# Performance work log

Measured on AMD Instinct MI355X. Metric: run time of the kernel, lower is better.

The kernel has to match this reference:

```python
import jax, jax.numpy as jnp
from jax import lax
import numpy as np

T, B, I, H, O = 1000, 256, 128, 512, 32
ALPHA = 20.0 / 100.0  # dt / tau
EXC_RATIO = 0.8
SPARSITY = 0.2


def setup_inputs() -> dict:
    key = jax.random.key(0)
    ks = jax.random.split(key, 8)
    x = jax.random.normal(ks[0], (T, B, I), dtype=jnp.float32)
    w_in = jax.random.normal(ks[1], (H, I), dtype=jnp.float32) * (1.0 / np.sqrt(I))
    b_in = jax.random.uniform(ks[2], (H,), dtype=jnp.float32, minval=-1, maxval=1) / np.sqrt(I)
    w_h = jax.random.normal(ks[3], (H, H), dtype=jnp.float32) * (1.0 / np.sqrt(H))
    b_h = jax.random.uniform(ks[4], (H,), dtype=jnp.float32, minval=-1, maxval=1) / np.sqrt(H)
    n_exc = int(H * EXC_RATIO)
    dale = jnp.where(jnp.arange(H) < n_exc, 1.0, -1.0).astype(jnp.float32)
    # sparse mask: rand < sparsity, diagonal forced True
    sp = (jax.random.uniform(ks[5], (H, H)) < SPARSITY).astype(jnp.float32)
    sparse = jnp.maximum(sp, jnp.eye(H, dtype=jnp.float32))
    fc_w = jax.random.normal(ks[6], (O, H), dtype=jnp.float32) * (1.0 / np.sqrt(H))
    fc_b = jax.random.uniform(ks[7], (O,), dtype=jnp.float32, minval=-1, maxval=1) / np.sqrt(H)
    return {"x": x, "w_in": w_in, "b_in": b_in, "w_h": w_h, "b_h": b_h,
            "dale": dale, "sparse": sparse, "fc_w": fc_w, "fc_b": fc_b}


def reference(x, w_in, b_in, w_h, b_h, dale, sparse, fc_w, fc_b):
    alpha = jnp.float32(ALPHA)
    oma = jnp.float32(1.0 - ALPHA)
    # effective recurrent weight: relu(W) * dale (per presynaptic column) * sparse mask
    w_eff = jax.nn.relu(w_h) * dale[None, :] * sparse  # [H, H]
    # precompute input drive for all timesteps: [T, B, H]
    x_drive = jnp.einsum('tbi,hi->tbh', x, w_in) + b_in

    def step(carry, xd_t):
        state, out = carry
        total = xd_t + out @ w_eff.T + b_h  # [B, H]
        state = state * oma + total * alpha
        out = jax.nn.relu(state)
        return (state, out), out

    init = (jnp.zeros((B, H), x.dtype), jnp.zeros((B, H), x.dtype))
    _, rnn_activity = lax.scan(step, init, x_drive)  # [T, B, H]
    out = jnp.einsum('tbh,oh->tbo', rnn_activity, fc_w) + fc_b  # [T, B, O]
    return out, rnn_activity
```

## Files before the change

### kernel.cpp

```cpp
#include <hip/hip_runtime.h>

#define T_STEPS 1000
#define BATCH   256
#define IN_DIM  128
#define HID     512
#define OUT_DIM 32
#define ALPHA_F 0.2f
#define OMA_F   0.8f
#define MAXNNZ  96


__global__ __launch_bounds__(512) void build_rank_kernel(
    const float* __restrict__ w_h, const float* __restrict__ sparse,
    unsigned int* __restrict__ perm, unsigned int* __restrict__ nnzR)
{
    int tid = threadIdx.x;
    __shared__ int cnt_sh[HID];

    const float4* wr4 = (const float4*)(w_h    + tid * HID);
    const float4* sr4 = (const float4*)(sparse + tid * HID);
    int cnt = 0;
    for (int j4 = 0; j4 < HID / 4; j4++) {
        float4 w = wr4[j4];
        float4 s = sr4[j4];
        if (w.x > 0.f && s.x > 0.5f) cnt++;
        if (w.y > 0.f && s.y > 0.5f) cnt++;
        if (w.z > 0.f && s.z > 0.5f) cnt++;
        if (w.w > 0.f && s.w > 0.5f) cnt++;
    }
    int c = min(cnt, MAXNNZ);

    cnt_sh[tid] = c;
    __syncthreads();
    int rank = 0;
    for (int j = 0; j < HID; j++) {
        int cj = cnt_sh[j];
        rank += (cj < c) || (cj == c && j < tid);
    }
    perm[rank] = (unsigned int)tid;
    nnzR[rank] = (unsigned int)c;
}

__global__ __launch_bounds__(64) void fill_kernel(
    const float* __restrict__ w_h, const float* __restrict__ dale,
    const float* __restrict__ sparse,
    const unsigned int* __restrict__ perm, const unsigned int* __restrict__ nnzR,
    float* __restrict__ val_t, unsigned short* __restrict__ idx_t)
{
    int r    = blockIdx.x;
    int lane = threadIdx.x;
    int h = (int)perm[r];
    int c = (int)nnzR[r];

    float*          vout = val_t + r * MAXNNZ;
    unsigned short* iout = idx_t + r * MAXNNZ;

    for (int k = lane; k < MAXNNZ; k += 64)
        if (k >= c) { vout[k] = 0.f; iout[k] = 0; }

    unsigned long long lt = (1ull << lane) - 1ull;
    int pos_base = 0;
#pragma unroll
    for (int ch = 0; ch < 8; ch++) {
        int j = ch * 64 + lane;
        float w = w_h[h * HID + j];
        float s = sparse[h * HID + j];
        bool pred = (w > 0.f) && (s > 0.5f);
        unsigned long long m = __ballot(pred);
        if (pred) {
            int pos = pos_base + (int)__popcll(m & lt);
            if (pos < MAXNNZ) {
                vout[pos] = w * dale[j];
                iout[pos] = (unsigned short)(j * 4);
            }
        }
        pos_base += (int)__popcll(m);
    }
}

__global__ __launch_bounds__(256) void trans_kernel(
    const float* __restrict__ w_in, const float* __restrict__ fc_w,
    float* __restrict__ w_inT, float* __restrict__ fcT)
{
    int o = blockIdx.x * 256 + threadIdx.x;
    if (o < IN_DIM * HID) {
        int k = o / HID, n = o % HID;
        w_inT[o] = w_in[n * IN_DIM + k];
    } else {
        int o2 = o - IN_DIM * HID;
        if (o2 < HID * OUT_DIM) {
            int k = o2 / OUT_DIM, oo = o2 % OUT_DIM;
            fcT[o2] = fc_w[oo * HID + k];
        }
    }
}

__global__ __launch_bounds__(256, 4) void ingemm_kernel(
    const float* __restrict__ x, const float* __restrict__ w_inT,
    const float* __restrict__ b_in, const float* __restrict__ b_h,
    float* __restrict__ xd)
{
    __shared__ float xl[256 * 33];
    int tid = threadIdx.x;
    int B  = blockIdx.x;
    int r8 = B & 7;
    int tt = B >> 3;
    int nc = tt & 15;
    int aa = tt >> 4;
    int mb = 8 * aa + r8;
    long m0 = (long)mb * 256;
    int n0 = nc * 32;

    float acc[32];
#pragma unroll
    for (int j = 0; j < 32; j++) acc[j] = b_in[n0 + j] + b_h[n0 + j];

    for (int k0 = 0; k0 < IN_DIM; k0 += 32) {
        __syncthreads();
#pragma unroll
        for (int i = 0; i < 8; i++) {
            int f  = tid + i * 256;
            int rr = f >> 3, cc = f & 7;
            float4 v = *(const float4*)(x + (m0 + rr) * IN_DIM + k0 + cc * 4);
            float* d = &xl[rr * 33 + cc * 4];
            d[0] = v.x; d[1] = v.y; d[2] = v.z; d[3] = v.w;
        }
        __syncthreads();
        const float* xrow = &xl[tid * 33];
#pragma unroll
        for (int kk = 0; kk < 32; kk++) {
            float a = xrow[kk];
            const float* wrow = w_inT + (k0 + kk) * HID + n0;
#pragma unroll
            for (int j = 0; j < 32; j++) acc[j] = fmaf(a, wrow[j], acc[j]);
        }
    }
    float* orow = xd + (m0 + tid) * HID + n0;
#pragma unroll
    for (int j = 0; j < 8; j++)
        *(float4*)(orow + j * 4) =
            make_float4(acc[4*j], acc[4*j+1], acc[4*j+2], acc[4*j+3]);
}


#define PAIR2(base, ii)                                              \
    {                                                                \
        unsigned int pk = idp[ii];                                   \
        float g0 = *(const float*)((base) + (pk & 0xffffu));         \
        float g1 = *(const float*)((base) + (pk >> 16));             \
        a0 = fmaf(val[2*(ii)],     g0, a0);                          \
        a1 = fmaf(val[2*(ii) + 1], g1, a1);                          \
    }

#define CHUNK2(base, c)                                              \
    PAIR2(base, 2*(c)+0) PAIR2(base, 2*(c)+1)

__device__ __forceinline__ float sparse_accum(
    const char* base, const float (&val)[MAXNNZ],
    const unsigned int (&idp)[MAXNNZ / 2], int nch, float a_init)
{
    float a0 = a_init, a1 = 0.f;
    switch (nch) {
        case 24: CHUNK2(base, 23) [[fallthrough]];
        case 23: CHUNK2(base, 22) [[fallthrough]];
        case 22: CHUNK2(base, 21) [[fallthrough]];
        case 21: CHUNK2(base, 20) [[fallthrough]];
        case 20: CHUNK2(base, 19) [[fallthrough]];
        case 19: CHUNK2(base, 18) [[fallthrough]];
        case 18: CHUNK2(base, 17) [[fallthrough]];
        case 17: CHUNK2(base, 16) [[fallthrough]];
        case 16: CHUNK2(base, 15) [[fallthrough]];
        case 15: CHUNK2(base, 14) [[fallthrough]];
        case 14: CHUNK2(base, 13) [[fallthrough]];
        case 13: CHUNK2(base, 12) [[fallthrough]];
        case 12: CHUNK2(base, 11) [[fallthrough]];
        case 11: CHUNK2(base, 10) [[fallthrough]];
        case 10: CHUNK2(base,  9) [[fallthrough]];
        case  9: CHUNK2(base,  8) [[fallthrough]];
        case  8: CHUNK2(base,  7) [[fallthrough]];
        case  7: CHUNK2(base,  6) [[fallthrough]];
        case  6: CHUNK2(base,  5) [[fallthrough]];
        case  5: CHUNK2(base,  4) [[fallthrough]];
        case  4: CHUNK2(base,  3) [[fallthrough]];
        case  3: CHUNK2(base,  2) [[fallthrough]];
        case  2: CHUNK2(base,  1) [[fallthrough]];
        case  1: CHUNK2(base,  0) break;
        default: break;
    }
    return a0 + a1;
}

__global__ __launch_bounds__(512, 2) void scan_kernel(
    float* __restrict__ act_g,
    const float* __restrict__ val_t, const unsigned short* __restrict__ idx_t,
    const unsigned int* __restrict__ perm, const unsigned int* __restrict__ nnzR)
{
    int tid = threadIdx.x;
    int b   = blockIdx.x;
    __shared__ float sbuf[1024];
    sbuf[tid] = 0.f;

    float        val[MAXNNZ];
    unsigned int idp[MAXNNZ / 2];
    {
        const float4* vp = (const float4*)(val_t + tid * MAXNNZ);
#pragma unroll
        for (int i = 0; i < MAXNNZ / 4; i++) {
            float4 v = vp[i];
            val[4*i] = v.x; val[4*i+1] = v.y; val[4*i+2] = v.z; val[4*i+3] = v.w;
        }
        const uint4* ip = (const uint4*)(idx_t + tid * MAXNNZ);
#pragma unroll
        for (int i = 0; i < MAXNNZ / 8; i++) {
            uint4 u = ip[i];
            idp[4*i] = u.x; idp[4*i+1] = u.y; idp[4*i+2] = u.z; idp[4*i+3] = u.w;
        }
    }
    int h = (int)perm[tid];
    int wmax = (int)nnzR[tid | 63];
    wmax = __builtin_amdgcn_readfirstlane(wmax);
    int nch = (wmax + 3) >> 2;

    float state = 0.f;
    int gi = b * HID + h;
    float xdv = act_g[gi];
    const char* sb = (const char*)sbuf;
    __syncthreads();

    for (int t = 0; t < T_STEPS; t += 2) {
        {
            float xn = act_g[gi + BATCH * HID];
            float a = sparse_accum(sb, val, idp, nch, xdv);
            state = state * OMA_F + a * ALPHA_F;
            float act = fmaxf(state, 0.f);
            sbuf[512 + h] = act;
            act_g[gi] = act;
            gi += BATCH * HID;
            xdv = xn;
            __syncthreads();
        }
        {
            int gn = (t < T_STEPS - 2) ? gi + BATCH * HID : gi;
            float xn = act_g[gn];
            float a = sparse_accum(sb + 2048, val, idp, nch, xdv);
            state = state * OMA_F + a * ALPHA_F;
            float act = fmaxf(state, 0.f);
            sbuf[h] = act;
            act_g[gi] = act;
            gi += BATCH * HID;
            xdv = xn;
            __syncthreads();
        }
    }
}

__global__ __launch_bounds__(256, 4) void outgemm_kernel(
    const float* __restrict__ act_g, const float* __restrict__ fcT,
    const float* __restrict__ fc_b, float* __restrict__ out_g)
{
    __shared__ float al[256 * 33];
    int tid = threadIdx.x;
    long m0 = (long)blockIdx.x * 256;

    float acc[32];
#pragma unroll
    for (int o = 0; o < 32; o++) acc[o] = fc_b[o];

    for (int k0 = 0; k0 < HID; k0 += 32) {
        __syncthreads();
#pragma unroll
        for (int i = 0; i < 8; i++) {
            int f  = tid + i * 256;
            int rr = f >> 3, cc = f & 7;
            float4 v = *(const float4*)(act_g + (m0 + rr) * HID + k0 + cc * 4);
            float* d = &al[rr * 33 + cc * 4];
            d[0] = v.x; d[1] = v.y; d[2] = v.z; d[3] = v.w;
        }
        __syncthreads();
        const float* arow = &al[tid * 33];
#pragma unroll
        for (int kk = 0; kk < 32; kk++) {
            float a = arow[kk];
            const float* frow = fcT + (k0 + kk) * OUT_DIM;
#pragma unroll
            for (int o = 0; o < 32; o++) acc[o] = fmaf(a, frow[o], acc[o]);
        }
    }
    float* orow = out_g + (m0 + tid) * OUT_DIM;
#pragma unroll
    for (int j = 0; j < 8; j++)
        *(float4*)(orow + j * 4) =
            make_float4(acc[4*j], acc[4*j+1], acc[4*j+2], acc[4*j+3]);
}

extern "C" void kernel_launch(void* const* d_in, const int* in_sizes, int n_in,
                              void* d_out, int out_size, void* d_ws, size_t ws_size,
                              hipStream_t stream)
{
    const float* x      = (const float*)d_in[0];
    const float* w_in   = (const float*)d_in[1];
    const float* b_in   = (const float*)d_in[2];
    const float* w_h    = (const float*)d_in[3];
    const float* b_h    = (const float*)d_in[4];
    const float* dale   = (const float*)d_in[5];
    const float* sparse = (const float*)d_in[6];
    const float* fc_w   = (const float*)d_in[7];
    const float* fc_b   = (const float*)d_in[8];

    float* out_g = (float*)d_out;
    float* act_g = out_g + (long)T_STEPS * BATCH * OUT_DIM;

    char* ws = (char*)d_ws;
    float*          val_t = (float*)(ws + 0);
    unsigned short* idx_t = (unsigned short*)(ws + 196608);
    unsigned int*   perm  = (unsigned int*)(ws + 294912);
    unsigned int*   nnzR  = (unsigned int*)(ws + 296960);
    float*          w_inT = (float*)(ws + 299008);
    float*          fcT   = (float*)(ws + 561152);

    build_rank_kernel<<<1, 512, 0, stream>>>(w_h, sparse, perm, nnzR);
    fill_kernel<<<HID, 64, 0, stream>>>(w_h, dale, sparse, perm, nnzR, val_t, idx_t);
    trans_kernel<<<320, 256, 0, stream>>>(w_in, fc_w, w_inT, fcT);
    ingemm_kernel<<<16000, 256, 0, stream>>>(x, w_inT, b_in, b_h, act_g);
    scan_kernel<<<256, 512, 0, stream>>>(act_g, val_t, idx_t, perm, nnzR);
    outgemm_kernel<<<1000, 256, 0, stream>>>(act_g, fcT, fc_b, out_g);
}
```

Baseline: 2.046 ms.

## Reorder sparse recurrent entries to avoid LDS bank conflicts in scan

Adds a preprocessing kernel that reorders each row's nonzero entries so that, at each step, the 32 lanes of a half-wavefront access distinct LDS banks (word & 31) when gathering the previous hidden state. Conflicting slots are padded with zero-valued dummy entries that point at unclaimed banks, and the per-row count is raised to the max schedule length in the wave. This targets LDS bank conflicts in the sequential scan's sparse matvec. In exchange, every row in a wave may do more iterations because of the padding, and a serial, heavily synchronised scheduling kernel is added to the setup.

```diff
diff --git a/kernel.cpp b/kernel.cpp
--- a/kernel.cpp
+++ b/kernel.cpp
@@ -8,6 +8,7 @@
 #define ALPHA_F 0.2f
 #define OMA_F   0.8f
 #define MAXNNZ  96
+#define BDEPTH  16
 
 
 __global__ __launch_bounds__(512) void build_rank_kernel(
@@ -75,6 +76,98 @@
             }
         }
         pos_base += (int)__popcll(m);
+    }
+}
+
+__global__ __launch_bounds__(64) void sched_kernel(
+    float* __restrict__ val_t, unsigned short* __restrict__ idx_t,
+    unsigned int* __restrict__ nnzR)
+{
+    int w    = blockIdx.x;
+    int lane = threadIdx.x;
+    int rank = w * 64 + lane;
+    int g    = lane >> 5;
+    int l32  = lane & 31;
+
+    __shared__ unsigned short entb[64][32][BDEPTH];
+    __shared__ unsigned char  cntb[64][32];
+    __shared__ unsigned char  outsrc[64][MAXNNZ];
+    __shared__ float          vll[64][MAXNNZ];
+    __shared__ unsigned int   claimed[2];
+    __shared__ int            lr[64];
+
+    int c = (int)nnzR[rank];
+
+    for (int b = 0; b < 32; b++) cntb[lane][b] = 0;
+    for (int e = 0; e < MAXNNZ; e++) {
+        vll[lane][e]    = val_t[rank * MAXNNZ + e];
+        outsrc[lane][e] = 255;
+    }
+    unsigned int bm = 0;
+    for (int e = 0; e < c; e++) {
+        int word = ((int)idx_t[rank * MAXNNZ + e]) >> 2;
+        int b = word & 31;
+        int k = cntb[lane][b];
+        if (k < BDEPTH) {
+            entb[lane][b][k] = (unsigned short)((e << 9) | word);
+            cntb[lane][b] = (unsigned char)(k + 1);
+            bm |= 1u << b;
+        }
+    }
+    __syncthreads();
+
+    int lastReal = -1;
+    int rem = c;
+    for (int s = 0; s < MAXNNZ; s++) {
+        if (__ballot(rem > 0) == 0ull) break;
+        if (lane == 0) { claimed[0] = 0; claimed[1] = 0; }
+        __syncthreads();
+        int placedWord = -1, placedSrc = -1;
+        for (int p = 0; p < 32; p++) {
+            if (l32 == p && rem > 0) {
+                unsigned int cl    = claimed[g];
+                unsigned int avail = bm & ~cl;
+                int b = -1;
+                if (avail)                    b = __ffs(avail) - 1;
+                else if (rem >= MAXNNZ - s)   b = __ffs(bm) - 1;
+                if (b >= 0) {
+                    int k = (int)cntb[lane][b] - 1;
+                    unsigned short pk = entb[lane][b][k];
+                    cntb[lane][b] = (unsigned char)k;
+                    if (k == 0) bm &= ~(1u << b);
+                    claimed[g] |= 1u << b;
+                    placedWord = pk & 511;
+                    placedSrc  = pk >> 9;
+                    rem--;
+                }
+            }
+            __syncthreads();
+        }
+        if (placedWord >= 0) {
+            idx_t[rank * MAXNNZ + s] = (unsigned short)(placedWord * 4);
+            outsrc[lane][s] = (unsigned char)placedSrc;
+            lastReal = s;
+        } else {
+            unsigned int freeb = ~claimed[g];
+            int pb = freeb ? (__ffs(freeb) - 1) : 0;
+            idx_t[rank * MAXNNZ + s] = (unsigned short)(pb * 4);
+        }
+        __syncthreads();
+    }
+
+    lr[lane] = lastReal;
+    __syncthreads();
+    int S;
+    {
+        int m = -1;
+        for (int i = 0; i < 64; i++) m = max(m, lr[i]);
+        S = m + 1;
+    }
+    nnzR[rank] = (unsigned int)S;
+
+    for (int s = 0; s < MAXNNZ; s++) {
+        int src = outsrc[lane][s];
+        val_t[rank * MAXNNZ + s] = (src == 255) ? 0.f : vll[lane][src];
     }
 }
 
@@ -320,6 +413,7 @@
 
     build_rank_kernel<<<1, 512, 0, stream>>>(w_h, sparse, perm, nnzR);
     fill_kernel<<<HID, 64, 0, stream>>>(w_h, dale, sparse, perm, nnzR, val_t, idx_t);
+    sched_kernel<<<8, 64, 0, stream>>>(val_t, idx_t, nnzR);
     trans_kernel<<<320, 256, 0, stream>>>(w_in, fc_w, w_inT, fcT);
     ingemm_kernel<<<16000, 256, 0, stream>>>(x, w_inT, b_in, b_h, act_g);
     scan_kernel<<<256, 512, 0, stream>>>(act_g, val_t, idx_t, perm, nnzR);
```

New measurement: 2.612 ms. 27.7% more time.
